# Kernel tuning notes

Hardware: AMD Instinct MI355X
Metric: run time of the kernel (lower is better)

The kernel has to match this reference:

```python
import jax, jax.numpy as jnp
import numpy as np

H = 16  # n_heads
D = 1024  # embed_dim == input_dim
FF = 4 * D
EPS = 1e-5  # torch LayerNorm default


def layer_norm(x, g, b):
    m = x.mean(-1, keepdims=True)
    v = x.var(-1, keepdims=True)
    return (x - m) / jnp.sqrt(v + EPS) * g + b


def setup_inputs() -> dict:
    key = jax.random.key(0)
    ks = jax.random.split(key, 8)
    s = lambda k, sh: (jax.random.normal(k, sh, jnp.float32) * 0.02)
    return {
        "kq": jax.random.normal(ks[0], (4, 2048, 512), jnp.float32),
        "v": jax.random.normal(ks[1], (4, 2048, 512), jnp.float32),
        "Wk": s(ks[2], (D, D)), "bk": jnp.zeros((D,), jnp.float32),
        "Wq": s(ks[3], (D, D)), "bq": jnp.zeros((D,), jnp.float32),
        "Wv": s(ks[4], (D, D)), "bv": jnp.zeros((D,), jnp.float32),
        "W1": s(ks[5], (FF, D)), "b1": jnp.zeros((FF,), jnp.float32),
        "W2": s(ks[6], (D, FF)), "b2": jnp.zeros((D,), jnp.float32),
        "g1": jnp.ones((D,), jnp.float32), "be1": jnp.zeros((D,), jnp.float32),
        "g2": jnp.ones((D,), jnp.float32), "be2": jnp.zeros((D,), jnp.float32),
    }


def reference(kq, v, Wk, bk, Wq, bq, Wv, bv, W1, b1, W2, b2, g1, be1, g2, be2):
    X = jnp.concatenate([kq, v], axis=-1)  # [n, T, input_dim]
    n, T, _ = kq.shape

    def heads(y):  # [n, T, D] -> [n, H, T, hd]
        return y.reshape(n, T, H, -1).transpose(0, 2, 1, 3)

    K = heads(X @ Wk.T + bk)
    Q = heads(X @ Wq.T + bq)
    V = heads(X @ Wv.T + bv)

    # NOTE: source applies no 1/sqrt(head_dim) scaling
    scores = jnp.einsum('nhqd,nhkd->nhqk', Q, K)
    causal = jnp.tril(jnp.ones((T, T), bool))  # mask = -inf strictly above diagonal
    scores = jnp.where(causal, scores, -jnp.inf)
    A = jax.nn.softmax(scores, axis=-1)
    attn_out = jnp.einsum('nhqk,nhkd->nhqd', A, V)
    attn_out = attn_out.transpose(0, 2, 1, 3).reshape(n, T, -1)  # [n, T, D]

    Vflat = V.transpose(0, 2, 1, 3).reshape(n, T, -1)  # residual is V projection, per source
    h = layer_norm(Vflat + attn_out, g1, be1)
    ff = jax.nn.gelu(h @ W1.T + b1, approximate=False) @ W2.T + b2  # torch GELU default = exact erf
    return layer_norm(h + ff, g2, be2)
```

## Files before the change

kernel.cpp:

```cpp
#include <hip/hip_runtime.h>
#include <stdint.h>

#define SEQ 2048
#define DM  1024
#define NH  16
#define HD  64
#define FFD 4096
#define TOK 8192

typedef __bf16 bf16x8 __attribute__((ext_vector_type(8)));
typedef float  f32x4  __attribute__((ext_vector_type(4)));
typedef float  f32x16 __attribute__((ext_vector_type(16)));
typedef unsigned short u16x8 __attribute__((ext_vector_type(8)));
typedef unsigned short u16x4 __attribute__((ext_vector_type(4)));
typedef unsigned int   u32x4 __attribute__((ext_vector_type(4)));

__device__ __forceinline__ unsigned short f2bf(float f) {
  unsigned u = __builtin_bit_cast(unsigned, f);
  u += 0x7fffu + ((u >> 16) & 1u);
  return (unsigned short)(u >> 16);
}
__device__ __forceinline__ float bf2f(unsigned short h) {
  return __builtin_bit_cast(float, ((unsigned)h) << 16);
}
__device__ __forceinline__ f32x4 mfma16(bf16x8 a, bf16x8 b, f32x4 c) {
  return __builtin_amdgcn_mfma_f32_16x16x32_bf16(a, b, c, 0, 0, 0);
}
__device__ __forceinline__ f32x16 mfma32(bf16x8 a, bf16x8 b, f32x16 c) {
  return __builtin_amdgcn_mfma_f32_32x32x16_bf16(a, b, c, 0, 0, 0);
}
__device__ __forceinline__ unsigned cvtpk(float lo, float hi) {
  unsigned r;
  asm("v_cvt_pk_bf16_f32 %0, %1, %2" : "=v"(r) : "v"(lo), "v"(hi));
  return r;
}
__device__ __forceinline__ void gld_lds16(void* lds, const void* g) {
  __builtin_amdgcn_global_load_lds((__attribute__((address_space(1))) void*)g,
                                   (__attribute__((address_space(3))) void*)lds,
                                   16, 0, 0);
}

__global__ __launch_bounds__(256) void concat_cast(
    const float* __restrict__ kq, const float* __restrict__ v,
    unsigned short* __restrict__ X) {
  int i = (blockIdx.x * 256 + threadIdx.x) * 4;
  int tkn = i >> 10;
  int c = i & 1023;
  const float* s = (c < 512) ? (kq + (size_t)tkn * 512 + c)
                             : (v  + (size_t)tkn * 512 + (c - 512));
  f32x4 f = *(const f32x4*)s;
  u16x4 o = { f2bf(f[0]), f2bf(f[1]), f2bf(f[2]), f2bf(f[3]) };
  *(u16x4*)&X[i] = o;
}

__global__ __launch_bounds__(256) void cast_f2b(
    const float* __restrict__ src, unsigned short* __restrict__ dst, int n) {
  int i = (blockIdx.x * 256 + threadIdx.x) * 4;
  if (i >= n) return;
  f32x4 f = *(const f32x4*)&src[i];
  u16x4 o = { f2bf(f[0]), f2bf(f[1]), f2bf(f[2]), f2bf(f[3]) };
  *(u16x4*)&dst[i] = o;
}

template<int EPI>
__global__ __launch_bounds__(512, 2) void gemm256(
    const unsigned short* __restrict__ A, const unsigned short* __restrict__ B,
    const float* __restrict__ bias, void* __restrict__ Cout,
    int M, int N, int K) {
  extern __shared__ __align__(16) unsigned short lds[];
  unsigned short* Asm0 = lds;
  unsigned short* Bsm0 = lds + 2 * 256 * 64;
  const int tid = threadIdx.x;
  const int w = tid >> 6, l = tid & 63, lr = l & 15, lg = l >> 4;
  const int wm = w >> 2, wn = w & 3;
  const int nbm = M >> 8;
  const int cpx = gridDim.x >> 3;
  const int bid = blockIdx.x;
  const int sw = (bid & 7) * cpx + (bid >> 3);
  const int bm = (sw % nbm) << 8;
  const int bn = (sw / nbm) << 8;
  const int NT = K >> 6;
  const int srow = tid >> 3;
  const int sc8  = tid & 7;

  f32x4 acc[8][4] = {};

  auto stage = [&](int kt, int bb) {
    unsigned short* da = Asm0 + bb * (256 * 64);
    unsigned short* db = Bsm0 + bb * (256 * 64);
#pragma unroll
    for (int i = 0; i < 4; ++i) {
      int row = i * 64 + srow;
      int c8s = (sc8 ^ (row & 7)) << 3;
      gld_lds16(da + (i * 512 + w * 64) * 8, &A[(size_t)(bm + row) * K + kt * 64 + c8s]);
      gld_lds16(db + (i * 512 + w * 64) * 8, &B[(size_t)(bn + row) * K + kt * 64 + c8s]);
    }
  };

  stage(0, 0);

  for (int t = 0; t < NT; ++t) {
    asm volatile("s_waitcnt vmcnt(0)" ::: "memory");
    __builtin_amdgcn_s_barrier();
    if (t + 1 < NT) stage(t + 1, (t + 1) & 1);
    const unsigned short* As = Asm0 + (t & 1) * (256 * 64);
    const unsigned short* Bs = Bsm0 + (t & 1) * (256 * 64);
    bf16x8 bv[4][2];
#pragma unroll
    for (int fn = 0; fn < 4; ++fn)
#pragma unroll
      for (int kk = 0; kk < 2; ++kk) {
        int row = wn * 64 + fn * 16 + lr;
        int c8 = (kk * 4 + lg) ^ (row & 7);
        bv[fn][kk] = *(const bf16x8*)&Bs[row * 64 + c8 * 8];
      }
#pragma unroll
    for (int mg = 0; mg < 2; ++mg) {
      bf16x8 av[4][2];
#pragma unroll
      for (int fr = 0; fr < 4; ++fr)
#pragma unroll
        for (int kk = 0; kk < 2; ++kk) {
          int row = wm * 128 + (mg * 4 + fr) * 16 + lr;
          int c8 = (kk * 4 + lg) ^ (row & 7);
          av[fr][kk] = *(const bf16x8*)&As[row * 64 + c8 * 8];
        }
      __builtin_amdgcn_s_setprio(1);
#pragma unroll
      for (int fr = 0; fr < 4; ++fr)
#pragma unroll
        for (int fn = 0; fn < 4; ++fn)
#pragma unroll
          for (int kk = 0; kk < 2; ++kk)
            acc[mg * 4 + fr][fn] = mfma16(av[fr][kk], bv[fn][kk], acc[mg * 4 + fr][fn]);
      __builtin_amdgcn_s_setprio(0);
    }
  }
#pragma unroll
  for (int mf = 0; mf < 8; ++mf) {
    int row0 = bm + wm * 128 + mf * 16 + lg * 4;
#pragma unroll
    for (int nf = 0; nf < 4; ++nf) {
      int col = bn + wn * 64 + nf * 16 + lr;
      float bcol = bias[col];
#pragma unroll
      for (int r = 0; r < 4; ++r) {
        float vv = acc[mf][nf][r] + bcol;
        int row = row0 + r;
        if (EPI == 2) vv = 0.5f * vv * (1.0f + erff(vv * 0.70710678118654752f));
        if (EPI == 0)
          ((float*)Cout)[(size_t)row * N + col] = vv;
        else if (EPI == 3) {
          int bb = row >> 11, t = row & 2047;
          int hh = col >> 6, dc = (col >> 4) & 3, dl = col & 15;
          ((unsigned short*)Cout)[((((size_t)(bb * 16 + hh) * 4 + dc) * 2048 + t) << 4) + dl] = f2bf(vv);
        } else
          ((unsigned short*)Cout)[(size_t)row * N + col] = f2bf(vv);
      }
    }
  }
}

__global__ __launch_bounds__(256) void vtrans_kernel(
    const unsigned short* __restrict__ Vb, unsigned short* __restrict__ VI) {
  __shared__ __align__(16) unsigned short T[64][72];
  const int tid = threadIdx.x;
  const int bh = blockIdx.x;
  const int b = bh >> 4, h = bh & 15;
  const int t0 = blockIdx.y * 64;
  const int m = tid & 7;
  const int rr = tid >> 3;
#pragma unroll
  for (int cc = 0; cc < 2; ++cc) {
    int tt = rr + cc * 32;
    u16x8 vv = *(const u16x8*)&Vb[((size_t)b * SEQ + t0 + tt) * DM + h * 64 + m * 8];
    *(u16x8*)&T[tt][(m ^ (tt >> 3)) * 8] = vv;
  }
  __syncthreads();
#pragma unroll
  for (int cc = 0; cc < 2; ++cc) {
    int d = rr + cc * 32;
    u16x8 ov;
#pragma unroll
    for (int jj = 0; jj < 8; ++jj) {
      int tt = m * 8 + jj;
      ov[jj] = T[tt][((d >> 3) ^ (tt >> 3)) * 8 + (d & 7)];
    }
    int kt = (t0 >> 4) + (m >> 1);
    *(u16x8*)&VI[(((size_t)bh * 128 + kt) * 64 + d) * 16 + (m & 1) * 8] = ov;
  }
}

__global__ __launch_bounds__(128, 4) void attn_kernel(
    const unsigned short* __restrict__ Q, const unsigned short* __restrict__ KI,
    const unsigned short* __restrict__ VI, unsigned short* __restrict__ O) {
  __shared__ __align__(16) unsigned short T[2][32 * 72];
  const int tid = threadIdx.x;
  const int w = tid >> 6, l = tid & 63;
  const int q32 = l & 31;
  const int g = l >> 5;
  const int x = blockIdx.x;
  const int bh = (x & 7) * 8 + (x >> 3);
  const int b = bh >> 4, h = bh & 15;
  const int u = 63 - (2 * (int)blockIdx.y + w);
  const size_t tok0 = (size_t)b * SEQ;
  const size_t hoff = (size_t)h * 64;
  const unsigned short* Kp = KI + (size_t)bh * 4 * SEQ * 16;
  const unsigned short* Vp = VI + (size_t)bh * 128 * 64 * 16;

  const int q0 = u * 32;
  const int qg = q0 + q32;

  bf16x8 qf[4];
#pragma unroll
  for (int ks = 0; ks < 4; ++ks)
    qf[ks] = *(const bf16x8*)&Q[(tok0 + qg) * DM + hoff + ks * 16 + g * 8];

  f32x16 ot0 = {}, ot1 = {};
  float m = -3.0e38f, lden = 0.f;

  bf16x8 kf[4], vf[4];
#pragma unroll
  for (int ks = 0; ks < 4; ++ks)
    kf[ks] = *(const bf16x8*)&Kp[((size_t)ks * SEQ + q32) * 16 + g * 8];
#pragma unroll
  for (int dt = 0; dt < 2; ++dt)
#pragma unroll
    for (int s = 0; s < 2; ++s)
      vf[dt * 2 + s] = *(const bf16x8*)&Vp[((size_t)s * 64 + dt * 32 + q32) * 16 + g * 8];

#pragma unroll 1
  for (int j = 0; j <= u; ++j) {
    f32x16 st = {};
    __builtin_amdgcn_s_setprio(1);
#pragma unroll
    for (int ks = 0; ks < 4; ++ks) st = mfma32(kf[ks], qf[ks], st);
    __builtin_amdgcn_s_setprio(0);
    const int jn = (j < u) ? j + 1 : u;
    bf16x8 kn[4], vn[4];
#pragma unroll
    for (int ks = 0; ks < 4; ++ks)
      kn[ks] = *(const bf16x8*)&Kp[((size_t)ks * SEQ + jn * 32 + q32) * 16 + g * 8];
#pragma unroll
    for (int dt = 0; dt < 2; ++dt)
#pragma unroll
      for (int s = 0; s < 2; ++s)
        vn[dt * 2 + s] = *(const bf16x8*)&Vp[(((size_t)jn * 2 + s) * 64 + dt * 32 + q32) * 16 + g * 8];
    if (j == u) {
#pragma unroll
      for (int r = 0; r < 16; ++r) {
        int kg = j * 32 + (r & 3) + 8 * (r >> 2) + 4 * g;
        if (kg > qg) st[r] = -3.0e38f;
      }
    }
    float x0 = fmaxf(st[0], st[1]),  x1 = fmaxf(st[2], st[3]);
    float x2 = fmaxf(st[4], st[5]),  x3 = fmaxf(st[6], st[7]);
    float x4 = fmaxf(st[8], st[9]),  x5 = fmaxf(st[10], st[11]);
    float x6 = fmaxf(st[12], st[13]), x7 = fmaxf(st[14], st[15]);
    x0 = fmaxf(x0, x1); x2 = fmaxf(x2, x3); x4 = fmaxf(x4, x5); x6 = fmaxf(x6, x7);
    x0 = fmaxf(x0, x2); x4 = fmaxf(x4, x6);
    float pmax = fmaxf(x0, x4);
    if (__any(pmax - m > 8.0f)) {
      float pp = fmaxf(pmax, __shfl_xor(pmax, 32, 64));
      float mnew = fmaxf(m, pp);
      float sc = __expf(m - mnew);
#pragma unroll
      for (int r = 0; r < 16; ++r) { ot0[r] *= sc; ot1[r] *= sc; }
      lden *= sc;
      m = mnew;
    }
    float p[16];
#pragma unroll
    for (int r = 0; r < 16; ++r) p[r] = __expf(st[r] - m);
    {
      float s0 = p[0] + p[1], s1 = p[2] + p[3], s2 = p[4] + p[5], s3 = p[6] + p[7];
      float s4 = p[8] + p[9], s5 = p[10] + p[11], s6 = p[12] + p[13], s7 = p[14] + p[15];
      s0 += s1; s2 += s3; s4 += s5; s6 += s7;
      s0 += s2; s4 += s6;
      lden += s0 + s4;
    }
    unsigned c0 = cvtpk(p[0], p[1]),   c1 = cvtpk(p[2], p[3]);
    unsigned c2 = cvtpk(p[4], p[5]),   c3 = cvtpk(p[6], p[7]);
    unsigned c4 = cvtpk(p[8], p[9]),   c5 = cvtpk(p[10], p[11]);
    unsigned c6 = cvtpk(p[12], p[13]), c7 = cvtpk(p[14], p[15]);
    unsigned y0 = __shfl_xor(c0, 32, 64), y1 = __shfl_xor(c1, 32, 64);
    unsigned y2 = __shfl_xor(c2, 32, 64), y3 = __shfl_xor(c3, 32, 64);
    unsigned y4 = __shfl_xor(c4, 32, 64), y5 = __shfl_xor(c5, 32, 64);
    unsigned y6 = __shfl_xor(c6, 32, 64), y7 = __shfl_xor(c7, 32, 64);
    u32x4 f0 = { g ? y2 : c0, g ? y3 : c1, g ? c2 : y0, g ? c3 : y1 };
    u32x4 f1 = { g ? y6 : c4, g ? y7 : c5, g ? c6 : y4, g ? c7 : y5 };
    bf16x8 pb0 = __builtin_bit_cast(bf16x8, f0);
    bf16x8 pb1 = __builtin_bit_cast(bf16x8, f1);
    __builtin_amdgcn_s_setprio(1);
    ot0 = mfma32(vf[0], pb0, ot0);
    ot0 = mfma32(vf[1], pb1, ot0);
    ot1 = mfma32(vf[2], pb0, ot1);
    ot1 = mfma32(vf[3], pb1, ot1);
    __builtin_amdgcn_s_setprio(0);
#pragma unroll
    for (int ks = 0; ks < 4; ++ks) kf[ks] = kn[ks];
#pragma unroll
    for (int q = 0; q < 4; ++q) vf[q] = vn[q];
  }
  lden += __shfl_xor(lden, 32, 64);
  float inv = 1.0f / lden;
#pragma unroll
  for (int r = 0; r < 16; ++r) {
    int d = (r & 3) + 8 * (r >> 2) + 4 * g;
    T[w][q32 * 72 + d]      = f2bf(ot0[r] * inv);
    T[w][q32 * 72 + 32 + d] = f2bf(ot1[r] * inv);
  }
#pragma unroll
  for (int j2 = 0; j2 < 4; ++j2) {
    int col = g * 32 + j2 * 8;
    u16x8 vv = *(const u16x8*)&T[w][q32 * 72 + col];
    *(u16x8*)&O[(tok0 + q0 + q32) * DM + hoff + col] = vv;
  }
}

template<int MODE>
__global__ __launch_bounds__(256) void ln_kernel(
    const unsigned short* __restrict__ Xa, const void* __restrict__ Xc,
    const float* __restrict__ g, const float* __restrict__ be,
    void* __restrict__ outp) {
  const int row = blockIdx.x, t = threadIdx.x;
  const size_t base = (size_t)row * DM + t * 4;
  float x[4];
  u16x4 a = *(const u16x4*)&Xa[base];
  if (MODE == 0) {
    u16x4 c = *(const u16x4*)&((const unsigned short*)Xc)[base];
#pragma unroll
    for (int i = 0; i < 4; ++i) x[i] = bf2f(a[i]) + bf2f(c[i]);
  } else {
    f32x4 c = *(const f32x4*)&((const float*)Xc)[base];
#pragma unroll
    for (int i = 0; i < 4; ++i) x[i] = bf2f(a[i]) + c[i];
  }
  float s = x[0] + x[1] + x[2] + x[3];
  float ss = x[0] * x[0] + x[1] * x[1] + x[2] * x[2] + x[3] * x[3];
#pragma unroll
  for (int m = 1; m < 64; m <<= 1) {
    s  += __shfl_xor(s, m, 64);
    ss += __shfl_xor(ss, m, 64);
  }
  __shared__ float red[8];
  const int w = t >> 6;
  if ((t & 63) == 0) { red[w * 2] = s; red[w * 2 + 1] = ss; }
  __syncthreads();
  s  = red[0] + red[2] + red[4] + red[6];
  ss = red[1] + red[3] + red[5] + red[7];
  const float mean = s * (1.0f / DM);
  const float var = ss * (1.0f / DM) - mean * mean;
  const float rstd = rsqrtf(var + 1e-5f);
  if (MODE == 0) {
    u16x4 o;
#pragma unroll
    for (int i = 0; i < 4; ++i) {
      int cx = t * 4 + i;
      o[i] = f2bf((x[i] - mean) * rstd * g[cx] + be[cx]);
    }
    *(u16x4*)&((unsigned short*)outp)[base] = o;
  } else {
    f32x4 o;
#pragma unroll
    for (int i = 0; i < 4; ++i) {
      int cx = t * 4 + i;
      o[i] = (x[i] - mean) * rstd * g[cx] + be[cx];
    }
    *(f32x4*)&((float*)outp)[base] = o;
  }
}

extern "C" void kernel_launch(void* const* d_in, const int* in_sizes, int n_in,
                              void* d_out, int out_size, void* d_ws, size_t ws_size,
                              hipStream_t stream) {
  (void)in_sizes; (void)n_in; (void)out_size; (void)ws_size;
  const float* kq  = (const float*)d_in[0];
  const float* v   = (const float*)d_in[1];
  const float* Wk  = (const float*)d_in[2];
  const float* bk  = (const float*)d_in[3];
  const float* Wq  = (const float*)d_in[4];
  const float* bq  = (const float*)d_in[5];
  const float* Wv  = (const float*)d_in[6];
  const float* bv  = (const float*)d_in[7];
  const float* W1  = (const float*)d_in[8];
  const float* b1  = (const float*)d_in[9];
  const float* W2  = (const float*)d_in[10];
  const float* b2  = (const float*)d_in[11];
  const float* g1  = (const float*)d_in[12];
  const float* be1 = (const float*)d_in[13];
  const float* g2  = (const float*)d_in[14];
  const float* be2 = (const float*)d_in[15];
  float* out = (float*)d_out;
  uint8_t* ws = (uint8_t*)d_ws;

  unsigned short* Xb  = (unsigned short*)(ws + 0);
  unsigned short* Wkb = (unsigned short*)(ws + 16777216);
  unsigned short* Wqb = (unsigned short*)(ws + 18874368);
  unsigned short* Wvb = (unsigned short*)(ws + 20971520);
  unsigned short* Qb  = (unsigned short*)(ws + 23068672);
  unsigned short* Kb  = (unsigned short*)(ws + 39845888);
  unsigned short* Ab  = (unsigned short*)(ws + 56623104);
  unsigned short* F1b = (unsigned short*)(ws + 0);
  unsigned short* W1b = (unsigned short*)(ws + 73400320);
  unsigned short* W2b = (unsigned short*)(ws + 81788928);
  unsigned short* Vb  = (unsigned short*)(ws + 90177536);
  unsigned short* Hb  = (unsigned short*)(ws + 106954752);
  float*          F2f = (float*)(ws + 123731968);
  unsigned short* VIg = (unsigned short*)(ws + 123731968);

  concat_cast<<<TOK * DM / 1024, 256, 0, stream>>>(kq, v, Xb);
  cast_f2b<<<1024, 256, 0, stream>>>(Wk, Wkb, DM * DM);
  cast_f2b<<<1024, 256, 0, stream>>>(Wq, Wqb, DM * DM);
  cast_f2b<<<1024, 256, 0, stream>>>(Wv, Wvb, DM * DM);
  cast_f2b<<<4096, 256, 0, stream>>>(W1, W1b, FFD * DM);
  cast_f2b<<<4096, 256, 0, stream>>>(W2, W2b, DM * FFD);

  gemm256<3><<<128, 512, 131072, stream>>>(Xb, Wkb, bk, Kb, TOK, DM, DM);
  gemm256<1><<<128, 512, 131072, stream>>>(Xb, Wqb, bq, Qb, TOK, DM, DM);
  gemm256<1><<<128, 512, 131072, stream>>>(Xb, Wvb, bv, Vb, TOK, DM, DM);

  vtrans_kernel<<<dim3(64, 32), 256, 0, stream>>>(Vb, VIg);
  attn_kernel<<<dim3(64, 32), 128, 0, stream>>>(Qb, Kb, VIg, Ab);

  ln_kernel<0><<<TOK, 256, 0, stream>>>(Vb, Ab, g1, be1, Hb);

  gemm256<2><<<512, 512, 131072, stream>>>(Hb, W1b, b1, F1b, TOK, FFD, DM);
  gemm256<0><<<128, 512, 131072, stream>>>(F1b, W2b, b2, F2f, TOK, DM, FFD);

  ln_kernel<1><<<TOK, 256, 0, stream>>>(Hb, F2f, g2, be2, out);
}
```

Baseline: 427.0 us.

## Fuse QKV projections into one GEMM with V-transpose epilogue and XCD patch scheduling

Relies on the Wk, Wq and Wv bf16 copies sitting contiguously so that a single 8192x3072 GEMM can compute K, Q and V in one launch. A concatenated bias buffer is built for it, and the epilogue writes K in its interleaved layout, Q row-major, and V both row-major and in the transposed VI layout, which removes the separate vtrans kernel. The GEMM is templated on BM (128 or 256), and a new XCD-aware patch mapping assigns contiguous tile patches to each XCD for better L2 reuse. The W2 GEMM moves to 128-row tiles to get 256 blocks instead of 128, giving better CU fill at the cost of lower per-block reuse. The scattered VI stores in the epilogue may be poorly coalesced.

```diff
diff --git a/kernel.cpp b/kernel.cpp
--- a/kernel.cpp
+++ b/kernel.cpp
@@ -62,38 +62,55 @@
   *(u16x4*)&dst[i] = o;
 }
 
-template<int EPI>
+__global__ __launch_bounds__(256) void bias3(
+    const float* __restrict__ a, const float* __restrict__ b,
+    const float* __restrict__ c, float* __restrict__ o) {
+  int i = blockIdx.x * 256 + threadIdx.x;
+  if (i < 1024) o[i] = a[i];
+  else if (i < 2048) o[i] = b[i - 1024];
+  else if (i < 3072) o[i] = c[i - 2048];
+}
+
+template<int BM, int EPI>
 __global__ __launch_bounds__(512, 2) void gemm256(
     const unsigned short* __restrict__ A, const unsigned short* __restrict__ B,
     const float* __restrict__ bias, void* __restrict__ Cout,
-    int M, int N, int K) {
+    void* __restrict__ CoutQ, void* __restrict__ CoutV, void* __restrict__ CoutVI,
+    int M, int N, int K, int PR, int PC, int NPC) {
+  constexpr int MF = BM / 32;
+  constexpr int MG = MF / 4;
   extern __shared__ __align__(16) unsigned short lds[];
   unsigned short* Asm0 = lds;
-  unsigned short* Bsm0 = lds + 2 * 256 * 64;
+  unsigned short* Bsm0 = lds + 2 * BM * 64;
   const int tid = threadIdx.x;
   const int w = tid >> 6, l = tid & 63, lr = l & 15, lg = l >> 4;
   const int wm = w >> 2, wn = w & 3;
-  const int nbm = M >> 8;
-  const int cpx = gridDim.x >> 3;
   const int bid = blockIdx.x;
-  const int sw = (bid & 7) * cpx + (bid >> 3);
-  const int bm = (sw % nbm) << 8;
-  const int bn = (sw / nbm) << 8;
+  const int xcd = bid & 7;
+  const int i = bid >> 3;
+  const int patch_r = xcd / NPC, patch_c = xcd % NPC;
+  const int bm = (patch_r * PR + (i % PR)) * BM;
+  const int bn = (patch_c * PC + (i / PR)) * 256;
   const int NT = K >> 6;
   const int srow = tid >> 3;
   const int sc8  = tid & 7;
 
-  f32x4 acc[8][4] = {};
+  f32x4 acc[MF][4] = {};
 
   auto stage = [&](int kt, int bb) {
-    unsigned short* da = Asm0 + bb * (256 * 64);
+    unsigned short* da = Asm0 + bb * (BM * 64);
     unsigned short* db = Bsm0 + bb * (256 * 64);
 #pragma unroll
-    for (int i = 0; i < 4; ++i) {
-      int row = i * 64 + srow;
-      int c8s = (sc8 ^ (row & 7)) << 3;
-      gld_lds16(da + (i * 512 + w * 64) * 8, &A[(size_t)(bm + row) * K + kt * 64 + c8s]);
-      gld_lds16(db + (i * 512 + w * 64) * 8, &B[(size_t)(bn + row) * K + kt * 64 + c8s]);
+    for (int p = 0; p < BM / 64; ++p) {
+      int row = p * 64 + srow;
+      gld_lds16(da + (p * 512 + w * 64) * 8,
+                &A[(size_t)(bm + row) * K + kt * 64 + ((sc8 ^ (row & 7)) << 3)]);
+    }
+#pragma unroll
+    for (int p = 0; p < 4; ++p) {
+      int row = p * 64 + srow;
+      gld_lds16(db + (p * 512 + w * 64) * 8,
+                &B[(size_t)(bn + row) * K + kt * 64 + ((sc8 ^ (row & 7)) << 3)]);
     }
   };
 
@@ -103,7 +120,7 @@
     asm volatile("s_waitcnt vmcnt(0)" ::: "memory");
     __builtin_amdgcn_s_barrier();
     if (t + 1 < NT) stage(t + 1, (t + 1) & 1);
-    const unsigned short* As = Asm0 + (t & 1) * (256 * 64);
+    const unsigned short* As = Asm0 + (t & 1) * (BM * 64);
     const unsigned short* Bs = Bsm0 + (t & 1) * (256 * 64);
     bf16x8 bv[4][2];
 #pragma unroll
@@ -115,13 +132,13 @@
         bv[fn][kk] = *(const bf16x8*)&Bs[row * 64 + c8 * 8];
       }
 #pragma unroll
-    for (int mg = 0; mg < 2; ++mg) {
+    for (int mg = 0; mg < MG; ++mg) {
       bf16x8 av[4][2];
 #pragma unroll
       for (int fr = 0; fr < 4; ++fr)
 #pragma unroll
         for (int kk = 0; kk < 2; ++kk) {
-          int row = wm * 128 + (mg * 4 + fr) * 16 + lr;
+          int row = wm * (BM / 2) + (mg * 4 + fr) * 16 + lr;
           int c8 = (kk * 4 + lg) ^ (row & 7);
           av[fr][kk] = *(const bf16x8*)&As[row * 64 + c8 * 8];
         }
@@ -137,8 +154,8 @@
     }
   }
 #pragma unroll
-  for (int mf = 0; mf < 8; ++mf) {
-    int row0 = bm + wm * 128 + mf * 16 + lg * 4;
+  for (int mf = 0; mf < MF; ++mf) {
+    int row0 = bm + wm * (BM / 2) + mf * 16 + lg * 4;
 #pragma unroll
     for (int nf = 0; nf < 4; ++nf) {
       int col = bn + wn * 64 + nf * 16 + lr;
@@ -148,46 +165,27 @@
         float vv = acc[mf][nf][r] + bcol;
         int row = row0 + r;
         if (EPI == 2) vv = 0.5f * vv * (1.0f + erff(vv * 0.70710678118654752f));
-        if (EPI == 0)
+        if (EPI == 0) {
           ((float*)Cout)[(size_t)row * N + col] = vv;
-        else if (EPI == 3) {
-          int bb = row >> 11, t = row & 2047;
-          int hh = col >> 6, dc = (col >> 4) & 3, dl = col & 15;
-          ((unsigned short*)Cout)[((((size_t)(bb * 16 + hh) * 4 + dc) * 2048 + t) << 4) + dl] = f2bf(vv);
-        } else
+        } else if (EPI == 5) {
+          int third = col >> 10, c = col & 1023;
+          unsigned short hv = f2bf(vv);
+          int bb = row >> 11, tt = row & 2047;
+          if (third == 0) {
+            int hh = c >> 6, dc = (c >> 4) & 3, dl = c & 15;
+            ((unsigned short*)Cout)[((((size_t)(bb * 16 + hh) * 4 + dc) * 2048 + tt) << 4) + dl] = hv;
+          } else if (third == 1) {
+            ((unsigned short*)CoutQ)[(size_t)row * 1024 + c] = hv;
+          } else {
+            ((unsigned short*)CoutV)[(size_t)row * 1024 + c] = hv;
+            int hh = c >> 6, d = c & 63;
+            ((unsigned short*)CoutVI)[((((size_t)(bb * 16 + hh) * 128 + (tt >> 4)) * 64 + d) << 4) + (tt & 15)] = hv;
+          }
+        } else {
           ((unsigned short*)Cout)[(size_t)row * N + col] = f2bf(vv);
+        }
       }
     }
-  }
-}
-
-__global__ __launch_bounds__(256) void vtrans_kernel(
-    const unsigned short* __restrict__ Vb, unsigned short* __restrict__ VI) {
-  __shared__ __align__(16) unsigned short T[64][72];
-  const int tid = threadIdx.x;
-  const int bh = blockIdx.x;
-  const int b = bh >> 4, h = bh & 15;
-  const int t0 = blockIdx.y * 64;
-  const int m = tid & 7;
-  const int rr = tid >> 3;
-#pragma unroll
-  for (int cc = 0; cc < 2; ++cc) {
-    int tt = rr + cc * 32;
-    u16x8 vv = *(const u16x8*)&Vb[((size_t)b * SEQ + t0 + tt) * DM + h * 64 + m * 8];
-    *(u16x8*)&T[tt][(m ^ (tt >> 3)) * 8] = vv;
-  }
-  __syncthreads();
-#pragma unroll
-  for (int cc = 0; cc < 2; ++cc) {
-    int d = rr + cc * 32;
-    u16x8 ov;
-#pragma unroll
-    for (int jj = 0; jj < 8; ++jj) {
-      int tt = m * 8 + jj;
-      ov[jj] = T[tt][((d >> 3) ^ (tt >> 3)) * 8 + (d & 7)];
-    }
-    int kt = (t0 >> 4) + (m >> 1);
-    *(u16x8*)&VI[(((size_t)bh * 128 + kt) * 64 + d) * 16 + (m & 1) * 8] = ov;
   }
 }
 
@@ -394,20 +392,21 @@
   float* out = (float*)d_out;
   uint8_t* ws = (uint8_t*)d_ws;
 
-  unsigned short* Xb  = (unsigned short*)(ws + 0);
-  unsigned short* Wkb = (unsigned short*)(ws + 16777216);
-  unsigned short* Wqb = (unsigned short*)(ws + 18874368);
-  unsigned short* Wvb = (unsigned short*)(ws + 20971520);
-  unsigned short* Qb  = (unsigned short*)(ws + 23068672);
-  unsigned short* Kb  = (unsigned short*)(ws + 39845888);
-  unsigned short* Ab  = (unsigned short*)(ws + 56623104);
-  unsigned short* F1b = (unsigned short*)(ws + 0);
-  unsigned short* W1b = (unsigned short*)(ws + 73400320);
-  unsigned short* W2b = (unsigned short*)(ws + 81788928);
-  unsigned short* Vb  = (unsigned short*)(ws + 90177536);
-  unsigned short* Hb  = (unsigned short*)(ws + 106954752);
-  float*          F2f = (float*)(ws + 123731968);
-  unsigned short* VIg = (unsigned short*)(ws + 123731968);
+  unsigned short* Xb   = (unsigned short*)(ws + 0);
+  unsigned short* Wkb  = (unsigned short*)(ws + 16777216);
+  unsigned short* Wqb  = (unsigned short*)(ws + 18874368);
+  unsigned short* Wvb  = (unsigned short*)(ws + 20971520);
+  unsigned short* Qb   = (unsigned short*)(ws + 23068672);
+  unsigned short* Kb   = (unsigned short*)(ws + 39845888);
+  unsigned short* Ab   = (unsigned short*)(ws + 56623104);
+  unsigned short* F1b  = (unsigned short*)(ws + 0);
+  unsigned short* W1b  = (unsigned short*)(ws + 73400320);
+  unsigned short* W2b  = (unsigned short*)(ws + 81788928);
+  unsigned short* Vb   = (unsigned short*)(ws + 90177536);
+  unsigned short* Hb   = (unsigned short*)(ws + 106954752);
+  float*          F2f  = (float*)(ws + 123731968);
+  unsigned short* VIg  = (unsigned short*)(ws + 123731968);
+  float*          bqkv = (float*)(ws + 140509184);
 
   concat_cast<<<TOK * DM / 1024, 256, 0, stream>>>(kq, v, Xb);
   cast_f2b<<<1024, 256, 0, stream>>>(Wk, Wkb, DM * DM);
@@ -415,18 +414,19 @@
   cast_f2b<<<1024, 256, 0, stream>>>(Wv, Wvb, DM * DM);
   cast_f2b<<<4096, 256, 0, stream>>>(W1, W1b, FFD * DM);
   cast_f2b<<<4096, 256, 0, stream>>>(W2, W2b, DM * FFD);
-
-  gemm256<3><<<128, 512, 131072, stream>>>(Xb, Wkb, bk, Kb, TOK, DM, DM);
-  gemm256<1><<<128, 512, 131072, stream>>>(Xb, Wqb, bq, Qb, TOK, DM, DM);
-  gemm256<1><<<128, 512, 131072, stream>>>(Xb, Wvb, bv, Vb, TOK, DM, DM);
-
-  vtrans_kernel<<<dim3(64, 32), 256, 0, stream>>>(Vb, VIg);
+  bias3<<<12, 256, 0, stream>>>(bk, bq, bv, bqkv);
+
+  gemm256<128, 5><<<768, 512, 98304, stream>>>(
+      Xb, Wkb, bqkv, Kb, Qb, Vb, VIg, TOK, 3072, DM, 8, 12, 1);
+
   attn_kernel<<<dim3(64, 32), 128, 0, stream>>>(Qb, Kb, VIg, Ab);
 
   ln_kernel<0><<<TOK, 256, 0, stream>>>(Vb, Ab, g1, be1, Hb);
 
-  gemm256<2><<<512, 512, 131072, stream>>>(Hb, W1b, b1, F1b, TOK, FFD, DM);
-  gemm256<0><<<128, 512, 131072, stream>>>(F1b, W2b, b2, F2f, TOK, DM, FFD);
+  gemm256<256, 2><<<512, 512, 131072, stream>>>(
+      Hb, W1b, b1, F1b, nullptr, nullptr, nullptr, TOK, FFD, DM, 8, 8, 2);
+  gemm256<128, 0><<<256, 512, 98304, stream>>>(
+      F1b, W2b, b2, F2f, nullptr, nullptr, nullptr, TOK, DM, FFD, 8, 4, 1);
 
   ln_kernel<1><<<TOK, 256, 0, stream>>>(Hb, F2f, g2, be2, out);
 }
```

After: 376.0 us. 1.14x faster.
